# Optimization experiments

Measured on AMD Instinct MI355X. Metric: run time of the kernel, lower is better.

Reference implementation:

```python
import math
import jax, jax.numpy as jnp
import numpy as np

K_VALUE = 2
CAPACITY_FACTOR_TRAIN = 1.25
MIN_CAPACITY = 4


def _get_capacity(s, e):
    capacity = math.floor(K_VALUE * CAPACITY_FACTOR_TRAIN * s / e)
    capacity += capacity % 2
    capacity = max(capacity, MIN_CAPACITY)
    return capacity


def setup_inputs() -> dict:
    key = jax.random.key(0)
    inputs = jax.random.normal(key, (8192, 8), dtype=jnp.float32)
    return {"inputs": inputs}


def reference(inputs):
    s, e = inputs.shape  # tokens, experts (static)
    capacity = _get_capacity(s, e)

    logits = jax.nn.softmax(inputs, axis=-1)  # [s, e]

    # top-1 / top-2 expert selection via masked argmax (matches torch argmax semantics)
    top1_idx = jnp.argmax(logits, axis=-1)  # [s]
    mask1 = jax.nn.one_hot(top1_idx, e, dtype=jnp.int32)  # [s, e]
    logits_except1 = jnp.where(mask1.astype(bool), -jnp.inf, logits)
    top2_idx = jnp.argmax(logits_except1, axis=-1)
    mask2 = jax.nn.one_hot(top2_idx, e, dtype=jnp.int32)

    # position-in-expert rank via exclusive cumsum over tokens (moe_cumsum = cumsum - 1)
    rank1 = jnp.cumsum(mask1, axis=0) - 1  # [s, e]
    rank2 = jnp.cumsum(mask2, axis=0) - 1 + jnp.sum(mask1, axis=0, keepdims=True)

    # drop tokens beyond capacity
    mask1 = mask1 * (rank1 < capacity).astype(jnp.int32)
    mask2 = mask2 * (rank2 < capacity).astype(jnp.int32)

    # scalar slot index per token
    rank1 = jnp.sum(mask1 * rank1, axis=-1)  # [s]
    rank2 = jnp.sum(mask2 * rank2, axis=-1)

    weight1 = mask1.astype(inputs.dtype) * logits  # [s, e]
    weight2 = mask2.astype(inputs.dtype) * logits

    rank1_sc = jax.nn.one_hot(rank1, capacity, dtype=inputs.dtype)  # [s, c]
    rank2_sc = jax.nn.one_hot(rank2, capacity, dtype=inputs.dtype)

    # combine weights: [s, e, c]
    cb_weight = weight1[:, :, None] * rank1_sc[:, None, :] + weight2[:, :, None] * rank2_sc[:, None, :]
    sec_mask = cb_weight.astype(bool)
    return cb_weight, sec_mask
```

## Files before the change

### kernel.cpp

```cpp
#include <hip/hip_runtime.h>
#include <hip/hip_bf16.h>
#include <stdint.h>


#define SCAN_THREADS 1024

__global__ __launch_bounds__(256) void top2_kernel(
    const float* __restrict__ in,
    float* __restrict__ w1o, float* __restrict__ w2o,
    unsigned char* __restrict__ eo, int s) {
  int t = blockIdx.x * blockDim.x + threadIdx.x;
  if (t >= s) return;
  const float4* p = reinterpret_cast<const float4*>(in + (size_t)t * 8);
  float4 a = p[0], b = p[1];
  float v[8] = {a.x, a.y, a.z, a.w, b.x, b.y, b.z, b.w};
  float m = v[0];
#pragma unroll
  for (int i = 1; i < 8; ++i) m = fmaxf(m, v[i]);
  float ex[8];
  float sum = 0.f;
#pragma unroll
  for (int i = 0; i < 8; ++i) { ex[i] = expf(v[i] - m); sum += ex[i]; }
  float inv = 1.0f / sum;
  int i1 = 0; float b1 = ex[0];
#pragma unroll
  for (int i = 1; i < 8; ++i) { if (ex[i] > b1) { b1 = ex[i]; i1 = i; } }
  int i2 = -1; float b2 = -1.f;
#pragma unroll
  for (int i = 0; i < 8; ++i) {
    if (i != i1 && ex[i] > b2) { b2 = ex[i]; i2 = i; }
  }
  w1o[t] = b1 * inv;
  w2o[t] = b2 * inv;
  eo[t] = (unsigned char)(i1 | (i2 << 3));
}

__global__ __launch_bounds__(SCAN_THREADS) void scan_kernel(
    const unsigned char* __restrict__ eo,
    short* __restrict__ slots,
    int s, int cap) {
  __shared__ int wave_cnt[SCAN_THREADS / 64][8];
  __shared__ int base[8];
  __shared__ int tot1[8];
  const int tid = threadIdx.x;
  const int lane = tid & 63;
  const int wave = tid >> 6;
  const unsigned long long lt =
      (lane == 0) ? 0ULL : (~0ULL >> (64 - lane));
  const int rounds = (s + SCAN_THREADS - 1) / SCAN_THREADS;

  if (tid < 8) base[tid] = 0;
  __syncthreads();

  for (int k = 0; k < rounds; ++k) {
    const int t = k * SCAN_THREADS + tid;
    int my = -1;
    if (t < s) my = eo[t] & 7;
    int lanepre = 0;
#pragma unroll
    for (int e = 0; e < 8; ++e) {
      unsigned long long bal = __ballot(my == e);
      if (lane == 0) wave_cnt[wave][e] = __popcll(bal);
      if (my == e) lanepre = __popcll(bal & lt);
    }
    __syncthreads();
    if (my >= 0) {
      int wavepre = 0;
      for (int w = 0; w < wave; ++w) wavepre += wave_cnt[w][my];
      int rank = base[my] + wavepre + lanepre;
      slots[2 * t] = (rank < cap) ? (short)rank : (short)-1;
    }
    __syncthreads();
    if (tid < 8) {
      int add = 0;
      for (int w = 0; w < SCAN_THREADS / 64; ++w) add += wave_cnt[w][tid];
      base[tid] += add;
    }
    __syncthreads();
  }
  if (tid < 8) { tot1[tid] = base[tid]; base[tid] = 0; }
  __syncthreads();

  for (int k = 0; k < rounds; ++k) {
    const int t = k * SCAN_THREADS + tid;
    int my = -1;
    if (t < s) my = (eo[t] >> 3) & 7;
    int lanepre = 0;
#pragma unroll
    for (int e = 0; e < 8; ++e) {
      unsigned long long bal = __ballot(my == e);
      if (lane == 0) wave_cnt[wave][e] = __popcll(bal);
      if (my == e) lanepre = __popcll(bal & lt);
    }
    __syncthreads();
    if (my >= 0) {
      int wavepre = 0;
      for (int w = 0; w < wave; ++w) wavepre += wave_cnt[w][my];
      int rank = base[my] + wavepre + lanepre + tot1[my];
      slots[2 * t + 1] = (rank < cap) ? (short)rank : (short)-1;
    }
    __syncthreads();
    if (tid < 8) {
      int add = 0;
      for (int w = 0; w < SCAN_THREADS / 64; ++w) add += wave_cnt[w][tid];
      base[tid] += add;
    }
    __syncthreads();
  }
}

__global__ __launch_bounds__(256) void fill_scatter_kernel(
    const float* __restrict__ w1, const float* __restrict__ w2,
    const unsigned char* __restrict__ eo, const short* __restrict__ slots,
    float* __restrict__ out, int s, int cap) {
  const int t = blockIdx.x;
  const int row = 8 * cap;
  float* cb = out + (size_t)t * row;
  float* mk = out + (size_t)s * row + (size_t)t * row;
  const float4 z = make_float4(0.f, 0.f, 0.f, 0.f);
  float4* cb4 = reinterpret_cast<float4*>(cb);
  float4* mk4 = reinterpret_cast<float4*>(mk);
  const int n4 = row / 4;
  for (int i = threadIdx.x; i < n4; i += 256) {
    cb4[i] = z;
    mk4[i] = z;
  }
  __syncthreads();
  if (threadIdx.x < 2) {
    const unsigned char p = eo[t];
    const int e = (threadIdx.x == 0) ? (p & 7) : ((p >> 3) & 7);
    const short sl = slots[2 * t + threadIdx.x];
    const float v = (threadIdx.x == 0) ? w1[t] : w2[t];
    if (sl >= 0) {
      const int pos = e * cap + (int)sl;
      cb[pos] = v;
      mk[pos] = (v != 0.f) ? 1.f : 0.f;
    }
  }
}

extern "C" void kernel_launch(void* const* d_in, const int* in_sizes, int n_in,
                              void* d_out, int out_size, void* d_ws, size_t ws_size,
                              hipStream_t stream) {
  const float* in = (const float*)d_in[0];
  const int E = 8;
  const int s = in_sizes[0] / E;
  int cap = (int)((5LL * s) / (2LL * E));
  cap += cap % 2;
  if (cap < 4) cap = 4;

  float* w1 = (float*)d_ws;
  float* w2 = w1 + s;
  unsigned char* eo = (unsigned char*)(w2 + s);
  short* slots = (short*)((((uintptr_t)(eo + s)) + 15) & ~(uintptr_t)15);

  top2_kernel<<<(s + 255) / 256, 256, 0, stream>>>(in, w1, w2, eo, s);
  scan_kernel<<<1, SCAN_THREADS, 0, stream>>>(eo, slots, s, cap);
  fill_scatter_kernel<<<s, 256, 0, stream>>>(w1, w2, eo, slots, (float*)d_out, s, cap);
}
```

Before: 1.331 ms.

## Fuse softmax top-2 with single-pass scan; split zero-fill and sparse scatter

Merges the softmax/top-2 selection into the single-block scan kernel and scans both expert choices in one pass, keeping per-token state in registers instead of two sequential scans through global memory. Output zeroing moves to a grid-stride fill kernel over the whole output, launched before the router so it need not wait on the scan. A separate scatter kernel writes the two nonzero entries per token from a compact float4 table. The cost is higher register use in the 1024-thread router block, and the design assumes s <= 8192 (ROUNDS fixed at 8).

```diff
diff --git a/kernel.cpp b/kernel.cpp
--- a/kernel.cpp
+++ b/kernel.cpp
@@ -3,140 +3,114 @@
 #include <stdint.h>
 
 
-#define SCAN_THREADS 1024
+#define ST 1024
+#define ROUNDS 8
 
-__global__ __launch_bounds__(256) void top2_kernel(
-    const float* __restrict__ in,
-    float* __restrict__ w1o, float* __restrict__ w2o,
-    unsigned char* __restrict__ eo, int s) {
-  int t = blockIdx.x * blockDim.x + threadIdx.x;
-  if (t >= s) return;
-  const float4* p = reinterpret_cast<const float4*>(in + (size_t)t * 8);
-  float4 a = p[0], b = p[1];
-  float v[8] = {a.x, a.y, a.z, a.w, b.x, b.y, b.z, b.w};
-  float m = v[0];
-#pragma unroll
-  for (int i = 1; i < 8; ++i) m = fmaxf(m, v[i]);
-  float ex[8];
-  float sum = 0.f;
-#pragma unroll
-  for (int i = 0; i < 8; ++i) { ex[i] = expf(v[i] - m); sum += ex[i]; }
-  float inv = 1.0f / sum;
-  int i1 = 0; float b1 = ex[0];
-#pragma unroll
-  for (int i = 1; i < 8; ++i) { if (ex[i] > b1) { b1 = ex[i]; i1 = i; } }
-  int i2 = -1; float b2 = -1.f;
-#pragma unroll
-  for (int i = 0; i < 8; ++i) {
-    if (i != i1 && ex[i] > b2) { b2 = ex[i]; i2 = i; }
-  }
-  w1o[t] = b1 * inv;
-  w2o[t] = b2 * inv;
-  eo[t] = (unsigned char)(i1 | (i2 << 3));
-}
-
-__global__ __launch_bounds__(SCAN_THREADS) void scan_kernel(
-    const unsigned char* __restrict__ eo,
-    short* __restrict__ slots,
-    int s, int cap) {
-  __shared__ int wave_cnt[SCAN_THREADS / 64][8];
-  __shared__ int base[8];
-  __shared__ int tot1[8];
+__global__ __launch_bounds__(ST) void router_kernel(
+    const float* __restrict__ in, float4* __restrict__ table, int s, int cap) {
+  __shared__ int wc1[ST / 64][8], wc2[ST / 64][8];
+  __shared__ int base1[8], base2[8];
   const int tid = threadIdx.x;
   const int lane = tid & 63;
   const int wave = tid >> 6;
-  const unsigned long long lt =
-      (lane == 0) ? 0ULL : (~0ULL >> (64 - lane));
-  const int rounds = (s + SCAN_THREADS - 1) / SCAN_THREADS;
+  const unsigned long long lt = (lane == 0) ? 0ULL : (~0ULL >> (64 - lane));
 
-  if (tid < 8) base[tid] = 0;
+  if (tid < 8) { base1[tid] = 0; base2[tid] = 0; }
   __syncthreads();
 
-  for (int k = 0; k < rounds; ++k) {
-    const int t = k * SCAN_THREADS + tid;
-    int my = -1;
-    if (t < s) my = eo[t] & 7;
-    int lanepre = 0;
+  int e1a[ROUNDS], e2a[ROUNDS], r1a[ROUNDS], r2a[ROUNDS];
+  float w1a[ROUNDS], w2a[ROUNDS];
+
+#pragma unroll
+  for (int k = 0; k < ROUNDS; ++k) {
+    const int t = k * ST + tid;
+    int e1 = -1, e2 = -1;
+    float w1 = 0.f, w2 = 0.f;
+    if (t < s) {
+      const float4* p = reinterpret_cast<const float4*>(in + (size_t)t * 8);
+      const float4 a = p[0], b = p[1];
+      float v[8] = {a.x, a.y, a.z, a.w, b.x, b.y, b.z, b.w};
+      float m = v[0];
+#pragma unroll
+      for (int i = 1; i < 8; ++i) m = fmaxf(m, v[i]);
+      float ex[8], sum = 0.f;
+#pragma unroll
+      for (int i = 0; i < 8; ++i) { ex[i] = expf(v[i] - m); sum += ex[i]; }
+      const float inv = 1.0f / sum;
+      e1 = 0; float b1 = v[0];
+#pragma unroll
+      for (int i = 1; i < 8; ++i) { if (v[i] > b1) { b1 = v[i]; e1 = i; } }
+      float b2 = -1e38f; e2 = 0;
+#pragma unroll
+      for (int i = 0; i < 8; ++i) {
+        if (i != e1 && v[i] > b2) { b2 = v[i]; e2 = i; }
+      }
+      w1 = ex[e1] * inv;
+      w2 = ex[e2] * inv;
+    }
+    int lp1 = 0, lp2 = 0;
 #pragma unroll
     for (int e = 0; e < 8; ++e) {
-      unsigned long long bal = __ballot(my == e);
-      if (lane == 0) wave_cnt[wave][e] = __popcll(bal);
-      if (my == e) lanepre = __popcll(bal & lt);
+      const unsigned long long m1 = __ballot(e1 == e);
+      const unsigned long long m2 = __ballot(e2 == e);
+      if (lane == 0) { wc1[wave][e] = __popcll(m1); wc2[wave][e] = __popcll(m2); }
+      if (e1 == e) lp1 = __popcll(m1 & lt);
+      if (e2 == e) lp2 = __popcll(m2 & lt);
     }
     __syncthreads();
-    if (my >= 0) {
-      int wavepre = 0;
-      for (int w = 0; w < wave; ++w) wavepre += wave_cnt[w][my];
-      int rank = base[my] + wavepre + lanepre;
-      slots[2 * t] = (rank < cap) ? (short)rank : (short)-1;
+    int r1 = 0, r2 = 0;
+    if (t < s) {
+      int wp1 = 0, wp2 = 0;
+      for (int w = 0; w < wave; ++w) { wp1 += wc1[w][e1]; wp2 += wc2[w][e2]; }
+      r1 = base1[e1] + wp1 + lp1;
+      r2 = base2[e2] + wp2 + lp2;
     }
     __syncthreads();
     if (tid < 8) {
-      int add = 0;
-      for (int w = 0; w < SCAN_THREADS / 64; ++w) add += wave_cnt[w][tid];
-      base[tid] += add;
+      int a1 = 0, a2 = 0;
+      for (int w = 0; w < ST / 64; ++w) { a1 += wc1[w][tid]; a2 += wc2[w][tid]; }
+      base1[tid] += a1;
+      base2[tid] += a2;
     }
     __syncthreads();
+    e1a[k] = e1; e2a[k] = e2; r1a[k] = r1; r2a[k] = r2; w1a[k] = w1; w2a[k] = w2;
   }
-  if (tid < 8) { tot1[tid] = base[tid]; base[tid] = 0; }
-  __syncthreads();
 
-  for (int k = 0; k < rounds; ++k) {
-    const int t = k * SCAN_THREADS + tid;
-    int my = -1;
-    if (t < s) my = (eo[t] >> 3) & 7;
-    int lanepre = 0;
 #pragma unroll
-    for (int e = 0; e < 8; ++e) {
-      unsigned long long bal = __ballot(my == e);
-      if (lane == 0) wave_cnt[wave][e] = __popcll(bal);
-      if (my == e) lanepre = __popcll(bal & lt);
-    }
-    __syncthreads();
-    if (my >= 0) {
-      int wavepre = 0;
-      for (int w = 0; w < wave; ++w) wavepre += wave_cnt[w][my];
-      int rank = base[my] + wavepre + lanepre + tot1[my];
-      slots[2 * t + 1] = (rank < cap) ? (short)rank : (short)-1;
-    }
-    __syncthreads();
-    if (tid < 8) {
-      int add = 0;
-      for (int w = 0; w < SCAN_THREADS / 64; ++w) add += wave_cnt[w][tid];
-      base[tid] += add;
-    }
-    __syncthreads();
+  for (int k = 0; k < ROUNDS; ++k) {
+    const int t = k * ST + tid;
+    if (t >= s) continue;
+    const int p1 = (r1a[k] < cap) ? e1a[k] * cap + r1a[k] : -1;
+    const int rr2 = r2a[k] + base1[e2a[k]];
+    const int p2 = (rr2 < cap) ? e2a[k] * cap + rr2 : -1;
+    float4 rec;
+    rec.x = __int_as_float(p1);
+    rec.y = w1a[k];
+    rec.z = __int_as_float(p2);
+    rec.w = w2a[k];
+    table[t] = rec;
   }
 }
 
-__global__ __launch_bounds__(256) void fill_scatter_kernel(
-    const float* __restrict__ w1, const float* __restrict__ w2,
-    const unsigned char* __restrict__ eo, const short* __restrict__ slots,
-    float* __restrict__ out, int s, int cap) {
-  const int t = blockIdx.x;
-  const int row = 8 * cap;
+__global__ __launch_bounds__(256) void fill_kernel(float4* __restrict__ out,
+                                                   unsigned n4) {
+  unsigned i = blockIdx.x * 256u + threadIdx.x;
+  const unsigned stride = gridDim.x * 256u;
+  const float4 z = make_float4(0.f, 0.f, 0.f, 0.f);
+  for (; i < n4; i += stride) out[i] = z;
+}
+
+__global__ __launch_bounds__(256) void scatter_kernel(
+    const float4* __restrict__ table, float* __restrict__ out, int s, int row) {
+  const int t = blockIdx.x * 256 + threadIdx.x;
+  if (t >= s) return;
+  const float4 rec = table[t];
+  const int p1 = __float_as_int(rec.x);
+  const int p2 = __float_as_int(rec.z);
   float* cb = out + (size_t)t * row;
-  float* mk = out + (size_t)s * row + (size_t)t * row;
-  const float4 z = make_float4(0.f, 0.f, 0.f, 0.f);
-  float4* cb4 = reinterpret_cast<float4*>(cb);
-  float4* mk4 = reinterpret_cast<float4*>(mk);
-  const int n4 = row / 4;
-  for (int i = threadIdx.x; i < n4; i += 256) {
-    cb4[i] = z;
-    mk4[i] = z;
-  }
-  __syncthreads();
-  if (threadIdx.x < 2) {
-    const unsigned char p = eo[t];
-    const int e = (threadIdx.x == 0) ? (p & 7) : ((p >> 3) & 7);
-    const short sl = slots[2 * t + threadIdx.x];
-    const float v = (threadIdx.x == 0) ? w1[t] : w2[t];
-    if (sl >= 0) {
-      const int pos = e * cap + (int)sl;
-      cb[pos] = v;
-      mk[pos] = (v != 0.f) ? 1.f : 0.f;
-    }
-  }
+  float* mk = cb + (size_t)s * row;
+  if (p1 >= 0) { cb[p1] = rec.y; mk[p1] = (rec.y != 0.f) ? 1.f : 0.f; }
+  if (p2 >= 0) { cb[p2] = rec.w; mk[p2] = (rec.w != 0.f) ? 1.f : 0.f; }
 }
 
 extern "C" void kernel_launch(void* const* d_in, const int* in_sizes, int n_in,
@@ -148,13 +122,12 @@
   int cap = (int)((5LL * s) / (2LL * E));
   cap += cap % 2;
   if (cap < 4) cap = 4;
+  const int row = E * cap;
 
-  float* w1 = (float*)d_ws;
-  float* w2 = w1 + s;
-  unsigned char* eo = (unsigned char*)(w2 + s);
-  short* slots = (short*)((((uintptr_t)(eo + s)) + 15) & ~(uintptr_t)15);
+  float4* table = (float4*)d_ws;
 
-  top2_kernel<<<(s + 255) / 256, 256, 0, stream>>>(in, w1, w2, eo, s);
-  scan_kernel<<<1, SCAN_THREADS, 0, stream>>>(eo, slots, s, cap);
-  fill_scatter_kernel<<<s, 256, 0, stream>>>(w1, w2, eo, slots, (float*)d_out, s, cap);
+  const unsigned n4 = (unsigned)((size_t)out_size / 4);
+  fill_kernel<<<2048, 256, 0, stream>>>((float4*)d_out, n4);
+  router_kernel<<<1, ST, 0, stream>>>(in, table, s, cap);
+  scatter_kernel<<<(s + 255) / 256, 256, 0, stream>>>(table, (float*)d_out, s, row);
 }
```

Result: slower. 1.381 ms (+3.7%).
